# Performance work log

Hardware: AMD Instinct MI355X
Metric: run time of the kernel (lower is better)

The kernel has to match this reference:

```python
import jax, jax.numpy as jnp
import numpy as np

# static config matching init_kwargs
IN_SIZE = 128
OUT_SIZE = 128
KSIZE = 3
POS = 10
DIL = 1
B = 8
L = 8192


def setup_inputs() -> dict:
    key = jax.random.key(0)
    k1, k2, k3, k4, k5 = jax.random.split(key, 5)
    inputs = jax.random.normal(k1, (B, IN_SIZE, L), dtype=jnp.float32)
    connections = jax.random.randint(k2, (B, L), 0, L)  # indices into length axis
    mask = jax.random.randint(k3, (B, L), 0, 2).astype(bool)
    ch_in = (2 * IN_SIZE + POS) * KSIZE  # 798
    W = jax.random.normal(k4, (OUT_SIZE, ch_in), dtype=jnp.float32) / np.float32(np.sqrt(ch_in))
    b = jax.random.normal(k5, (OUT_SIZE,), dtype=jnp.float32) * 0.01
    return {"inputs": inputs, "connections": connections, "mask": mask, "W": W, "b": b}


def reference(inputs, connections, mask, W, b):
    Bn, C, Ln = inputs.shape
    # gather neighbor features: out[b,c,l] = inputs[b,c,connections[b,l]]  -> [B,C,L]
    conn_vals = jnp.take_along_axis(inputs, connections[:, None, :], axis=2)
    # trig positional encoding of relative offsets  -> [B,POS,L]
    pos = jnp.arange(Ln, dtype=jnp.float32)[None]              # [1,L]
    delta = (pos - connections.astype(jnp.float32))[:, None, :]  # [B,1,L]
    scales = (2.0 ** jnp.arange(POS, dtype=jnp.float32))[None, :, None]
    penc = jnp.sin(scales * delta / 1000.0)
    out = jnp.concatenate([inputs, conn_vals, penc], axis=1)   # [B, 2C+POS, L]
    # non-causal pad + unfold (window KSIZE, step 1); num windows == L
    pad = KSIZE * DIL // 2
    out = jnp.pad(out, ((0, 0), (0, 0), (pad, pad)))
    # build [B, Ch, KSIZE, L]: window k is out_padded[..., k : k+L]
    out = jnp.stack([out[..., k:k + Ln] for k in range(KSIZE)], axis=2)
    out = out.reshape(Bn, -1, Ln)                               # [B, Ch*KSIZE, L]
    # 1x1 conv == per-position GEMM
    y = jnp.einsum('oc,bcl->bol', W, out) + b[None, :, None]    # [B, OUT, L]
    return y * mask[:, None, :].astype(y.dtype)
```

## Files before the change

### kernel.cpp

```cpp
#include <hip/hip_runtime.h>
#include <math.h>

#define B_    8
#define C_    128
#define L_    8192
#define O_    128
#define POS_  10
#define CHIN  798
#define CH_   266
#define GSTR  128
#define NCH   9
#define TL2   256
#define G_ELEMS  ((size_t)B_ * L_ * GSTR)
#define WT_ELEMS ((size_t)3 * NCH * O_ * 32)

typedef _Float16 half8 __attribute__((ext_vector_type(8)));
typedef short short8 __attribute__((ext_vector_type(8)));
typedef float f32x4  __attribute__((ext_vector_type(4)));

__device__ __forceinline__ void detect_core(const uint4* __restrict__ m,
                                            int* __restrict__ mflag, int tid) {
    __shared__ int s[2];
    if (tid < 2) s[tid] = 0;
    __syncthreads();
    unsigned sub = 0, mid = 0;
    #pragma unroll
    for (int k = 0; k < 16; ++k) {
        uint4 w = m[tid + k * 256];
        sub |= (w.x | w.y | w.z | w.w) & 0xFFFFFF00u;
        mid |= (w.y | w.w) & 0x000000FFu;
    }
    unsigned long long bs = __ballot(sub != 0);
    unsigned long long bm = __ballot(mid != 0);
    if ((tid & 63) == 0) {
        if (bs) atomicOr(&s[0], 1);
        if (bm) atomicOr(&s[1], 1);
    }
    __syncthreads();
    if (tid == 0) mflag[0] = s[0] ? 1 : (s[1] ? 0 : 2);
}

__global__ void detect_kernel(const uint4* __restrict__ m, int* __restrict__ mflag) {
    detect_core(m, mflag, threadIdx.x);
}

__global__ __launch_bounds__(256, 4)
void prep_kernel(const float* __restrict__ inputs, const float* __restrict__ W,
                 const uint4* __restrict__ maskv,
                 _Float16* __restrict__ G, _Float16* __restrict__ Wt2,
                 int* __restrict__ mflag) {
    __shared__ float tile[64][65];
    const int bid = blockIdx.x;
    const int tid = threadIdx.x;

    if (bid == 2480) { detect_core(maskv, mflag, tid); return; }

    if (bid >= 2048) {
        int idx = (bid - 2048) * 256 + tid;
        int cc  = idx & 31;
        int o   = (idx >> 5) & 127;
        int tch = idx >> 12;
        int ch  = tch % 9;
        int t   = tch / 9;
        int cg  = ch * 32 + cc;
        Wt2[idx] = (cg < CH_) ? (_Float16)W[o * CHIN + 3 * cg + t] : (_Float16)0.f;
        return;
    }

    const int b  = bid & 7;
    const int r  = bid >> 3;
    const int c0 = (r & 1) * 64;
    const int l0 = (r >> 1) * 64;
    const int ty = tid >> 6, tx = tid & 63;

    #pragma unroll
    for (int it = 0; it < 16; ++it) {
        int cl = it * 4 + ty;
        tile[cl][tx] = inputs[((size_t)(b * C_ + c0 + cl)) * L_ + l0 + tx];
    }
    __syncthreads();
    const int cp = (tid & 31) * 2;
    const int lr = tid >> 5;
    #pragma unroll
    for (int it = 0; it < 8; ++it) {
        int ll = it * 8 + lr;
        _Float16 pair[2] = {(_Float16)tile[cp][ll], (_Float16)tile[cp + 1][ll]};
        *(unsigned*)&G[((size_t)(b * L_ + l0 + ll)) * GSTR + c0 + cp] = *(unsigned*)pair;
    }
}

__global__ __launch_bounds__(512, 2)
void k2_gemm(const _Float16* __restrict__ G, const _Float16* __restrict__ Wt2,
             const int* __restrict__ conn,
             const unsigned char* __restrict__ mask,
             const float* __restrict__ bias,
             float* __restrict__ out,
             const int* __restrict__ mflag_p) {
    __shared__ _Float16 Bs[8][66][40];
    __shared__ int conn_s[258];

    const int bid = blockIdx.x;
    const int b   = bid & 7;
    const int l0  = (bid >> 3) * TL2;
    const int tid  = threadIdx.x;
    const int wave = tid >> 6;
    const int lane = tid & 63;
    const int wo = wave & 1;
    const int wl = wave >> 1;
    const int g  = lane >> 4;
    const int ln = lane & 15;
    const int lw0 = l0 + wl * 64 - 1;

    const _Float16* gb = G + (size_t)b * L_ * GSTR;
    _Float16 (*bsw)[40] = Bs[wave];

    for (int j = tid; j < TL2 + 2; j += 512) {
        int l_ = l0 - 1 + j;
        conn_s[j] = ((unsigned)l_ < (unsigned)L_) ? conn[b * L_ + l_] : 0;
    }
    __syncthreads();

    auto bload = [&](int ch, int q) -> half8 {
        int cb = q & 3, j = q >> 2;
        int l_ = lw0 + j;
        half8 v = (half8)0;
        if ((unsigned)l_ < (unsigned)L_) {
            if (ch < 4) {
                v = *(const half8*)&gb[(size_t)l_ * GSTR + ch * 32 + cb * 8];
            } else if (ch < 8) {
                int cj = conn_s[wl * 64 + j];
                v = *(const half8*)&gb[(size_t)cj * GSTR + (ch - 4) * 32 + cb * 8];
            } else if (cb < 2) {
                float d = (float)(l_ - conn_s[wl * 64 + j]);
                _Float16 h[8];
                #pragma unroll
                for (int e = 0; e < 8; ++e) {
                    int p = cb * 8 + e;
                    h[e] = (p < POS_) ? (_Float16)sinf(((float)(1 << p)) * d / 1000.0f)
                                      : (_Float16)0.f;
                }
                v = *(half8*)h;
            }
        }
        return v;
    };

#define ALOADF(DST, CH) { _Pragma("unroll") for (int t_ = 0; t_ < 3; ++t_) \
        _Pragma("unroll") for (int m_ = 0; m_ < 4; ++m_) \
            DST[t_][m_] = *(const half8*)&Wt2[((size_t)((t_ * NCH + (CH)) * O_ + wo * 64 + m_ * 16 + ln)) * 32 + g * 8]; }

#define BLOADF(DST, CH) { _Pragma("unroll") for (int it_ = 0; it_ < 5; ++it_) { \
        int q_ = it_ * 64 + lane; \
        DST[it_] = (q_ < 264) ? bload((CH), q_) : (half8)0; } }

#define BWRITEF(SRC) { _Pragma("unroll") for (int it_ = 0; it_ < 5; ++it_) { \
        int q_ = it_ * 64 + lane; \
        if (q_ < 264) { int cb_ = q_ & 3, j_ = q_ >> 2; *(half8*)&bsw[j_][cb_ * 8] = SRC[it_]; } } }

#define COMPUTE(AUSE) { _Pragma("unroll") for (int t_ = 0; t_ < 3; ++t_) { \
        half8 bf_[4]; \
        _Pragma("unroll") for (int n_ = 0; n_ < 4; ++n_) \
            bf_[n_] = *(const half8*)&bsw[n_ * 16 + ln + t_][8 * g]; \
        _Pragma("unroll") for (int m_ = 0; m_ < 4; ++m_) \
            _Pragma("unroll") for (int n_ = 0; n_ < 4; ++n_) \
                acc[m_][n_] = __builtin_amdgcn_mfma_f32_16x16x32_f16(AUSE[t_][m_], bf_[n_], acc[m_][n_], 0, 0, 0); } }

    f32x4 acc[4][4];
    #pragma unroll
    for (int m = 0; m < 4; ++m)
        #pragma unroll
        for (int n = 0; n < 4; ++n) acc[m][n] = (f32x4)0.f;

    half8 A0[3][4], A1[3][4], B0[5], B1[5];
    ALOADF(A0, 0);
    BLOADF(B0, 0);

    for (int ch = 0; ch < NCH; ch += 2) {
        BWRITEF(B0);
        if (ch + 1 < NCH) { ALOADF(A1, ch + 1); BLOADF(B1, ch + 1); }
        COMPUTE(A0);
        if (ch + 1 < NCH) {
            BWRITEF(B1);
            if (ch + 2 < NCH) { ALOADF(A0, ch + 2); BLOADF(B0, ch + 2); }
            COMPUTE(A1);
        }
    }

    const int mflag = mflag_p[0];
    float mv[4];
    #pragma unroll
    for (int n = 0; n < 4; ++n) {
        int l = l0 + wl * 64 + n * 16 + ln;
        int idx = b * L_ + l;
        if (mflag == 1)      mv[n] = mask[idx] ? 1.f : 0.f;
        else if (mflag == 0) mv[n] = ((const int*)mask)[idx] ? 1.f : 0.f;
        else                 mv[n] = ((const int*)mask)[2 * idx] ? 1.f : 0.f;
    }
    #pragma unroll
    for (int m = 0; m < 4; ++m) {
        #pragma unroll
        for (int r = 0; r < 4; ++r) {
            int o = wo * 64 + m * 16 + g * 4 + r;
            float bo = bias[o];
            #pragma unroll
            for (int n = 0; n < 4; ++n) {
                int l = l0 + wl * 64 + n * 16 + ln;
                out[((size_t)(b * O_ + o)) * L_ + l] = (acc[m][n][r] + bo) * mv[n];
            }
        }
    }
#undef ALOADF
#undef BLOADF
#undef BWRITEF
#undef COMPUTE
}

__global__ __launch_bounds__(256, 2)
void cc_fallback_kernel(const float* __restrict__ inputs,
                        const int* __restrict__ conn,
                        const unsigned char* __restrict__ mask,
                        const float* __restrict__ W,
                        const float* __restrict__ bias,
                        float* __restrict__ out,
                        const int* __restrict__ mflag_p) {
    __shared__ int   conn_s[130];
    __shared__ float feat_s[16][132];
    __shared__ float Ws[48][136];

    const int b   = blockIdx.y;
    const int l0  = blockIdx.x * 128;
    const int tid = threadIdx.x;
    const int ot  = tid >> 4;
    const int lt  = tid & 15;
    const int o0  = ot * 8;
    const int ll  = lt * 8;

    for (int j = tid; j < 130; j += 256) {
        int lg = l0 - 1 + j;
        conn_s[j] = ((unsigned)lg < (unsigned)L_) ? conn[b * L_ + lg] : -1;
    }
    float acc[8][8];
    #pragma unroll
    for (int i = 0; i < 8; ++i)
        #pragma unroll
        for (int j = 0; j < 8; ++j) acc[i][j] = 0.f;

    const int tc = ot, tj = lt;
    for (int chunk = 0; chunk < 17; ++chunk) {
        const int CN  = (chunk < 16) ? 16 : POS_;
        const int cg0 = chunk * 16;
        const int col0 = 3 * cg0;
        __syncthreads();
        {
            const int nw = O_ * CN * 3;
            for (int idx = tid; idx < nw; idx += 256) {
                int o = idx & 127, kk = idx >> 7;
                Ws[kk][o] = W[o * CHIN + col0 + kk];
            }
        }
        if (chunk < 8) {
            const float* src = inputs + ((size_t)b * C_ + (cg0 + tc)) * L_;
            for (int j = tj; j < 130; j += 16) {
                int lg = l0 - 1 + j;
                feat_s[tc][j] = ((unsigned)lg < (unsigned)L_) ? src[lg] : 0.f;
            }
        } else if (chunk < 16) {
            const float* src = inputs + ((size_t)b * C_ + (cg0 - 128 + tc)) * L_;
            for (int j = tj; j < 130; j += 16) {
                int cj = conn_s[j];
                feat_s[tc][j] = (cj >= 0) ? src[cj] : 0.f;
            }
        } else if (tc < POS_) {
            const float sc = (float)(1 << tc);
            for (int j = tj; j < 130; j += 16) {
                int cj = conn_s[j];
                int lg = l0 - 1 + j;
                float v = 0.f;
                if (cj >= 0) v = sinf((sc * (float)(lg - cj)) / 1000.0f);
                feat_s[tc][j] = v;
            }
        }
        __syncthreads();
        for (int c = 0; c < CN; ++c) {
            float f[10];
            float4 fa = *(const float4*)&feat_s[c][ll];
            float4 fb = *(const float4*)&feat_s[c][ll + 4];
            float2 fc2 = *(const float2*)&feat_s[c][ll + 8];
            f[0]=fa.x; f[1]=fa.y; f[2]=fa.z; f[3]=fa.w;
            f[4]=fb.x; f[5]=fb.y; f[6]=fb.z; f[7]=fb.w;
            f[8]=fc2.x; f[9]=fc2.y;
            #pragma unroll
            for (int k = 0; k < 3; ++k) {
                const float* wrow = &Ws[c * 3 + k][o0];
                float4 wa = *(const float4*)&wrow[0];
                float4 wb = *(const float4*)&wrow[4];
                float w[8] = {wa.x, wa.y, wa.z, wa.w, wb.x, wb.y, wb.z, wb.w};
                #pragma unroll
                for (int oi = 0; oi < 8; ++oi)
                    #pragma unroll
                    for (int li = 0; li < 8; ++li)
                        acc[oi][li] = fmaf(w[oi], f[li + k], acc[oi][li]);
            }
        }
    }
    const int mflag = mflag_p[0];
    const int lbase = l0 + ll;
    float mv[8];
    #pragma unroll
    for (int li = 0; li < 8; ++li) {
        int idx = b * L_ + lbase + li;
        if (mflag == 1)      mv[li] = mask[idx] ? 1.f : 0.f;
        else if (mflag == 0) mv[li] = ((const int*)mask)[idx] ? 1.f : 0.f;
        else                 mv[li] = ((const int*)mask)[2 * idx] ? 1.f : 0.f;
    }
    #pragma unroll
    for (int oi = 0; oi < 8; ++oi) {
        float bo = bias[o0 + oi];
        float* dst = out + ((size_t)b * O_ + o0 + oi) * L_ + lbase;
        #pragma unroll
        for (int li = 0; li < 8; ++li) dst[li] = (acc[oi][li] + bo) * mv[li];
    }
}

extern "C" void kernel_launch(void* const* d_in, const int* in_sizes, int n_in,
                              void* d_out, int out_size, void* d_ws, size_t ws_size,
                              hipStream_t stream) {
    const float*         inputs = (const float*)d_in[0];
    const int*           conn   = (const int*)d_in[1];
    const unsigned char* mask   = (const unsigned char*)d_in[2];
    const float*         W      = (const float*)d_in[3];
    const float*         bias   = (const float*)d_in[4];
    float*               out    = (float*)d_out;

    const size_t g_bytes  = G_ELEMS * sizeof(_Float16);
    const size_t wt_bytes = WT_ELEMS * sizeof(_Float16);
    const size_t need     = g_bytes + wt_bytes + 64;

    if (ws_size < need) {
        int* mflag = (int*)d_ws;
        detect_kernel<<<1, 256, 0, stream>>>((const uint4*)mask, mflag);
        dim3 grid(L_ / 128, B_);
        cc_fallback_kernel<<<grid, 256, 0, stream>>>(inputs, conn, mask, W, bias, out, mflag);
        return;
    }

    _Float16* G     = (_Float16*)d_ws;
    _Float16* Wt2   = (_Float16*)((char*)d_ws + g_bytes);
    int*      mflag = (int*)((char*)d_ws + g_bytes + wt_bytes);

    prep_kernel<<<2481, 256, 0, stream>>>(inputs, W, (const uint4*)mask, G, Wt2, mflag);
    k2_gemm<<<256, 512, 0, stream>>>(G, Wt2, conn, mask, bias, out, mflag);
}
```

Before: 52.89 us.

## Share B tile across waves with double-buffered LDS and smaller blocks

The GEMM block shrinks from 512 to 256 threads covering 128 positions, and the grid grows from 256 to 512 blocks. The per-wave private B tiles become one block-shared tile of 132 positions in a double buffer, loaded cooperatively and guarded by __syncthreads. Before, each wave loaded its own 66-row halo, so waves covering different positions fetched overlapping neighbour rows. Sharing removes those redundant gathers and sine evaluations and gives more blocks per device, at the cost of block-wide barriers every chunk.

```diff
diff --git a/kernel.cpp b/kernel.cpp
--- a/kernel.cpp
+++ b/kernel.cpp
@@ -10,7 +10,7 @@
 #define CH_   266
 #define GSTR  128
 #define NCH   9
-#define TL2   256
+#define TL2   128
 #define G_ELEMS  ((size_t)B_ * L_ * GSTR)
 #define WT_ELEMS ((size_t)3 * NCH * O_ * 32)
 
@@ -89,15 +89,15 @@
     }
 }
 
-__global__ __launch_bounds__(512, 2)
+__global__ __launch_bounds__(256)
 void k2_gemm(const _Float16* __restrict__ G, const _Float16* __restrict__ Wt2,
              const int* __restrict__ conn,
              const unsigned char* __restrict__ mask,
              const float* __restrict__ bias,
              float* __restrict__ out,
              const int* __restrict__ mflag_p) {
-    __shared__ _Float16 Bs[8][66][40];
-    __shared__ int conn_s[258];
+    __shared__ _Float16 Bs[2][132][40];
+    __shared__ int conn_s[130];
 
     const int bid = blockIdx.x;
     const int b   = bid & 7;
@@ -109,29 +109,26 @@
     const int wl = wave >> 1;
     const int g  = lane >> 4;
     const int ln = lane & 15;
-    const int lw0 = l0 + wl * 64 - 1;
 
     const _Float16* gb = G + (size_t)b * L_ * GSTR;
-    _Float16 (*bsw)[40] = Bs[wave];
-
-    for (int j = tid; j < TL2 + 2; j += 512) {
+
+    for (int j = tid; j < TL2 + 2; j += 256) {
         int l_ = l0 - 1 + j;
         conn_s[j] = ((unsigned)l_ < (unsigned)L_) ? conn[b * L_ + l_] : 0;
     }
-    __syncthreads();
-
-    auto bload = [&](int ch, int q) -> half8 {
+
+    auto bload = [&](int ch, int q) -> short8 {
         int cb = q & 3, j = q >> 2;
-        int l_ = lw0 + j;
-        half8 v = (half8)0;
+        int l_ = l0 - 1 + j;
+        short8 v = (short8)0;
         if ((unsigned)l_ < (unsigned)L_) {
             if (ch < 4) {
-                v = *(const half8*)&gb[(size_t)l_ * GSTR + ch * 32 + cb * 8];
+                v = *(const short8*)&gb[(size_t)l_ * GSTR + ch * 32 + cb * 8];
             } else if (ch < 8) {
-                int cj = conn_s[wl * 64 + j];
-                v = *(const half8*)&gb[(size_t)cj * GSTR + (ch - 4) * 32 + cb * 8];
+                int cj = conn_s[j];
+                v = *(const short8*)&gb[(size_t)cj * GSTR + (ch - 4) * 32 + cb * 8];
             } else if (cb < 2) {
-                float d = (float)(l_ - conn_s[wl * 64 + j]);
+                float d = (float)(l_ - conn_s[j]);
                 _Float16 h[8];
                 #pragma unroll
                 for (int e = 0; e < 8; ++e) {
@@ -139,28 +136,30 @@
                     h[e] = (p < POS_) ? (_Float16)sinf(((float)(1 << p)) * d / 1000.0f)
                                       : (_Float16)0.f;
                 }
-                v = *(half8*)h;
+                v = *(short8*)h;
             }
         }
         return v;
     };
-
-#define ALOADF(DST, CH) { _Pragma("unroll") for (int t_ = 0; t_ < 3; ++t_) \
+    auto bwrite = [&](short8 s, int q, int buf) {
+        int cb = q & 3, j = q >> 2;
+        *(short8*)&Bs[buf][j][cb * 8] = s;
+    };
+
+#define ALOADR(DST, CH) { _Pragma("unroll") for (int t_ = 0; t_ < 3; ++t_) \
         _Pragma("unroll") for (int m_ = 0; m_ < 4; ++m_) \
             DST[t_][m_] = *(const half8*)&Wt2[((size_t)((t_ * NCH + (CH)) * O_ + wo * 64 + m_ * 16 + ln)) * 32 + g * 8]; }
 
-#define BLOADF(DST, CH) { _Pragma("unroll") for (int it_ = 0; it_ < 5; ++it_) { \
-        int q_ = it_ * 64 + lane; \
-        DST[it_] = (q_ < 264) ? bload((CH), q_) : (half8)0; } }
-
-#define BWRITEF(SRC) { _Pragma("unroll") for (int it_ = 0; it_ < 5; ++it_) { \
-        int q_ = it_ * 64 + lane; \
-        if (q_ < 264) { int cb_ = q_ & 3, j_ = q_ >> 2; *(half8*)&bsw[j_][cb_ * 8] = SRC[it_]; } } }
-
-#define COMPUTE(AUSE) { _Pragma("unroll") for (int t_ = 0; t_ < 3; ++t_) { \
+#define BLOADR(CH) { s0 = bload((CH), tid); s1 = bload((CH), tid + 256); \
+        if (tid < 8) s2 = bload((CH), 512 + tid); }
+
+#define BWR(BUF) { bwrite(s0, tid, (BUF)); bwrite(s1, tid + 256, (BUF)); \
+        if (tid < 8) bwrite(s2, 512 + tid, (BUF)); }
+
+#define COMPUTE(AUSE, BUF) { _Pragma("unroll") for (int t_ = 0; t_ < 3; ++t_) { \
         half8 bf_[4]; \
         _Pragma("unroll") for (int n_ = 0; n_ < 4; ++n_) \
-            bf_[n_] = *(const half8*)&bsw[n_ * 16 + ln + t_][8 * g]; \
+            bf_[n_] = *(const half8*)&Bs[BUF][wl * 64 + n_ * 16 + ln + t_][8 * g]; \
         _Pragma("unroll") for (int m_ = 0; m_ < 4; ++m_) \
             _Pragma("unroll") for (int n_ = 0; n_ < 4; ++n_) \
                 acc[m_][n_] = __builtin_amdgcn_mfma_f32_16x16x32_f16(AUSE[t_][m_], bf_[n_], acc[m_][n_], 0, 0, 0); } }
@@ -171,20 +170,28 @@
         #pragma unroll
         for (int n = 0; n < 4; ++n) acc[m][n] = (f32x4)0.f;
 
-    half8 A0[3][4], A1[3][4], B0[5], B1[5];
-    ALOADF(A0, 0);
-    BLOADF(B0, 0);
-
-    for (int ch = 0; ch < NCH; ch += 2) {
-        BWRITEF(B0);
-        if (ch + 1 < NCH) { ALOADF(A1, ch + 1); BLOADF(B1, ch + 1); }
-        COMPUTE(A0);
-        if (ch + 1 < NCH) {
-            BWRITEF(B1);
-            if (ch + 2 < NCH) { ALOADF(A0, ch + 2); BLOADF(B0, ch + 2); }
-            COMPUTE(A1);
-        }
-    }
+    half8 A0[3][4], A1[3][4];
+    short8 s0, s1, s2;
+
+    ALOADR(A0, 0);
+    BLOADR(0);
+    BWR(0);
+    __syncthreads();
+
+    for (int ch = 0; ch < 8; ch += 2) {
+        ALOADR(A1, ch + 1);
+        BLOADR(ch + 1);
+        COMPUTE(A0, 0);
+        BWR(1);
+        __syncthreads();
+
+        ALOADR(A0, ch + 2);
+        BLOADR(ch + 2);
+        COMPUTE(A1, 1);
+        BWR(0);
+        __syncthreads();
+    }
+    COMPUTE(A0, 0);
 
     const int mflag = mflag_p[0];
     float mv[4];
@@ -209,9 +216,9 @@
             }
         }
     }
-#undef ALOADF
-#undef BLOADF
-#undef BWRITEF
+#undef ALOADR
+#undef BLOADR
+#undef BWR
 #undef COMPUTE
 }
 
@@ -349,5 +356,5 @@
     int*      mflag = (int*)((char*)d_ws + g_bytes + wt_bytes);
 
     prep_kernel<<<2481, 256, 0, stream>>>(inputs, W, (const uint4*)mask, G, Wt2, mflag);
-    k2_gemm<<<256, 512, 0, stream>>>(G, Wt2, conn, mask, bias, out, mflag);
-}
+    k2_gemm<<<512, 256, 0, stream>>>(G, Wt2, conn, mask, bias, out, mflag);
+}
```

Result: faster. 49.35 us (-6.7%).
